# Optimization experiments

Hardware: AMD Instinct MI355X
Metric: run time of the kernel (lower is better)

The kernel has to match this reference:

```python
import jax, jax.numpy as jnp
import numpy as np

LAMBDA_TEMP = 20.0
GAMMA = 20.0
MARGIN = 0.05
EPS = 1e-8

B, K, M, D = 128, 256, 8, 128


def _unit(x, axis=-1):
    return x / jnp.linalg.norm(x, axis=axis, keepdims=True)


def setup_inputs() -> dict:
    key = jax.random.key(0)
    k1, k2, k3 = jax.random.split(key, 3)
    v_proj = _unit(jax.random.normal(k1, (B, K, D), dtype=jnp.float32))
    prototypes = _unit(jax.random.normal(k2, (K, M, D), dtype=jnp.float32))
    concept_labels = jax.random.randint(k3, (B, K), 0, 2, dtype=jnp.int64)
    return {"v_proj": v_proj, "concept_labels": concept_labels, "prototypes": prototypes}


def reference(v_proj, concept_labels, prototypes):
    # all-pairs prototype similarities: query vector (b,k) vs prototypes of concept c
    # sims: (B, K, C, M)
    sims = jnp.einsum('bkd,cmd->bkcm', v_proj, prototypes)
    # Eq.6: soft assignment over the M prototypes of each concept
    q = jax.nn.softmax(GAMMA * sims, axis=-1)
    # Eq.7-8: weighted similarity sim_c(v)  -> (B, K, C)
    sim = jnp.sum(q * sims, axis=-1)
    # positive similarity: concept k queried against its own prototypes, plus margin
    sim_pos = jnp.einsum('bkk->bk', sim) + MARGIN  # (B, K)
    # Eq.9: -log( exp(lam*sim_pos) / (sum_c exp(lam*sim_c) + eps) )
    denom = jnp.sum(jnp.exp(LAMBDA_TEMP * sim), axis=-1) + EPS  # (B, K)
    loss_bk = jnp.log(denom) - LAMBDA_TEMP * sim_pos  # (B, K)
    mask = (concept_labels == 1).astype(loss_bk.dtype)
    num_pos = jnp.sum(mask)
    total = jnp.sum(loss_bk * mask)
    return jnp.where(num_pos > 0, total / num_pos, total)
```

## Files before the change

kernel.cpp:

```cpp
#include <hip/hip_runtime.h>

#define NROWS 32768
#define LT 20.0f
#define CHUNKS 16

typedef _Float16 half8 __attribute__((ext_vector_type(8)));
typedef float    f32x4 __attribute__((ext_vector_type(4)));

__device__ __forceinline__ float swz16(float x) {
    return __int_as_float(__builtin_amdgcn_ds_swizzle(__float_as_int(x), 0x401F));
}

#define GLD16(gp, lp) __builtin_amdgcn_global_load_lds( \
    (const __attribute__((address_space(1))) void*)(gp), \
    (__attribute__((address_space(3))) void*)(lp), 16, 0, 0)

__global__ __launch_bounds__(256)
void mpcl_prep(const float* __restrict__ P, _Float16* __restrict__ Pw)
{
    int id   = blockIdx.x * 256 + threadIdx.x;
    int gcol = id >> 4;
    int dblk = id & 15;
    int ch   = gcol >> 7;
    int col  = gcol & 127;
    int key  = (col & 3) | ((col & 8) >> 1);
    int dbs  = (dblk & 8) | ((dblk ^ key) & 7);
    const float* src = P + (size_t)gcol * 128 + dblk * 8;
    float4 a = *(const float4*)src;
    float4 b = *(const float4*)(src + 4);
    half8 hv;
    hv[0] = (_Float16)a.x; hv[1] = (_Float16)a.y;
    hv[2] = (_Float16)a.z; hv[3] = (_Float16)a.w;
    hv[4] = (_Float16)b.x; hv[5] = (_Float16)b.y;
    hv[6] = (_Float16)b.z; hv[7] = (_Float16)b.w;
    *(half8*)&Pw[((size_t)ch * 2048 + col * 16 + dbs) * 8] = hv;
}

__global__ __launch_bounds__(1024)
void mpcl_main(const float* __restrict__ V,
               const int*   __restrict__ labels,
               const _Float16* __restrict__ Pw,
               int* __restrict__ ws,
               float* __restrict__ out)
{
    __shared__ __align__(16) _Float16 Pst[2][2048 * 8];
    __shared__ float sh_denom[128];
    __shared__ float sh_simpos[128];
    __shared__ float sh_red[32];

    int*   gcnt = ws;
    float* gsum = (float*)(ws + 2);

    const int tid  = threadIdx.x;
    const int lane = tid & 63;
    const int w    = tid >> 6;
    const int rg   = w >> 2;
    const int colq = w & 3;
    const int n    = lane & 15;
    const int q    = lane >> 4;
    const int rowbase = blockIdx.x * 128;

    if (tid < 128) { sh_denom[tid] = 0.0f; sh_simpos[tid] = 0.0f; }

    half8 vh[2][4];
#pragma unroll
    for (int rf = 0; rf < 2; ++rf) {
        const float* vr = V + (size_t)(rowbase + rg * 32 + rf * 16 + n) * 128 + q * 8;
#pragma unroll
        for (int c = 0; c < 4; ++c) {
            float4 x0 = *(const float4*)(vr + c * 32);
            float4 x1 = *(const float4*)(vr + c * 32 + 4);
            vh[rf][c][0] = (_Float16)x0.x; vh[rf][c][1] = (_Float16)x0.y;
            vh[rf][c][2] = (_Float16)x0.z; vh[rf][c][3] = (_Float16)x0.w;
            vh[rf][c][4] = (_Float16)x1.x; vh[rf][c][5] = (_Float16)x1.y;
            vh[rf][c][6] = (_Float16)x1.z; vh[rf][c][7] = (_Float16)x1.w;
        }
    }

    const int col1 = colq * 32 + ((n >> 2) << 3) + (n & 3);
    int off1[4];
#pragma unroll
    for (int c = 0; c < 4; ++c) {
        int dblk = c * 4 + q;
        int dbs  = (dblk & 8) | ((dblk ^ (n & 7)) & 7);
        off1[c]  = (col1 * 16 + dbs) * 8;
    }

    const _Float16* gbase = Pw + (size_t)(w * 128 + lane) * 8;
    _Float16* l0 = &Pst[0][(w * 128) * 8];
    _Float16* l1 = &Pst[1][(w * 128) * 8];

    GLD16(gbase,       l0);
    GLD16(gbase + 512, l0 + 512);

    const int rowk0 = (rowbase + rg * 32 + n) & 255;
    const int rowk1 = (rowbase + rg * 32 + 16 + n) & 255;

    float dn[2] = {0.f, 0.f};

#pragma unroll 1
    for (int ch = 0; ch < CHUNKS; ++ch) {
        __syncthreads();

        if (ch < CHUNKS - 1) {
            const _Float16* g = gbase + (size_t)(ch + 1) * 16384;
            _Float16* lnx = (ch & 1) ? l0 : l1;
            GLD16(g,       lnx);
            GLD16(g + 512, lnx + 512);
        }

        const _Float16* base = (ch & 1) ? &Pst[1][0] : &Pst[0][0];

        f32x4 acc1[2] = {{0.f,0.f,0.f,0.f},{0.f,0.f,0.f,0.f}};
        f32x4 acc2[2] = {{0.f,0.f,0.f,0.f},{0.f,0.f,0.f,0.f}};
#pragma unroll
        for (int c = 0; c < 4; ++c) {
            half8 a1 = *(const half8*)&base[off1[c]];
            half8 a2 = *(const half8*)&base[off1[c] + 512];
            acc1[0] = __builtin_amdgcn_mfma_f32_16x16x32_f16(a1, vh[0][c], acc1[0], 0, 0, 0);
            acc1[1] = __builtin_amdgcn_mfma_f32_16x16x32_f16(a1, vh[1][c], acc1[1], 0, 0, 0);
            acc2[0] = __builtin_amdgcn_mfma_f32_16x16x32_f16(a2, vh[0][c], acc2[0], 0, 0, 0);
            acc2[1] = __builtin_amdgcn_mfma_f32_16x16x32_f16(a2, vh[1][c], acc2[1], 0, 0, 0);
        }

        const int cA = ch * 16 + colq * 4 + q;
#pragma unroll
        for (int rf = 0; rf < 2; ++rf) {
            float x0 = acc1[rf][0], x1 = acc1[rf][1], x2 = acc1[rf][2], x3 = acc1[rf][3];
            float x4 = acc2[rf][0], x5 = acc2[rf][1], x6 = acc2[rf][2], x7 = acc2[rf][3];
            float e0 = __expf(LT * x0), e1 = __expf(LT * x1);
            float e2 = __expf(LT * x2), e3 = __expf(LT * x3);
            float e4 = __expf(LT * x4), e5 = __expf(LT * x5);
            float e6 = __expf(LT * x6), e7 = __expf(LT * x7);
            float es = ((e0 + e1) + (e2 + e3)) + ((e4 + e5) + (e6 + e7));
            float ss = fmaf(e0, x0, fmaf(e1, x1, fmaf(e2, x2, e3 * x3)))
                     + fmaf(e4, x4, fmaf(e5, x5, fmaf(e6, x6, e7 * x7)));
            float simc = __fdividef(ss, es);
            dn[rf] += __expf(LT * simc);
            if (cA == (rf ? rowk1 : rowk0))
                sh_simpos[rg * 32 + rf * 16 + n] = simc;
        }
    }

#pragma unroll
    for (int rf = 0; rf < 2; ++rf) {
        float t = dn[rf];
        t += swz16(t);
        t += __shfl_xor(t, 32);
        if (lane < 16)
            atomicAdd(&sh_denom[rg * 32 + rf * 16 + n], t);
    }
    __syncthreads();

    float s = 0.f, cc = 0.f;
    if (tid < 128) {
        int row = rowbase + tid;
        float lp = logf(sh_denom[tid] + 1e-8f) - LT * (sh_simpos[tid] + 0.05f);
        float mk = (labels[row] == 1) ? 1.0f : 0.0f;
        s = lp * mk;
        cc = mk;
    }
#pragma unroll
    for (int off = 32; off >= 1; off >>= 1) {
        s  += __shfl_down(s, off);
        cc += __shfl_down(cc, off);
    }
    if (lane == 0) { sh_red[w] = s; sh_red[16 + w] = cc; }
    __syncthreads();
    if (tid == 0) {
        s = 0.f; cc = 0.f;
#pragma unroll
        for (int i = 0; i < 16; ++i) { s += sh_red[i]; cc += sh_red[16 + i]; }
        atomicAdd(&gsum[0], s);
        atomicAdd(&gsum[1], cc);
        __threadfence();
        int g = __hip_atomic_fetch_add(gcnt, 1,
                                       __ATOMIC_ACQ_REL, __HIP_MEMORY_SCOPE_AGENT);
        if (g == 255) {
            __threadfence();
            float ts = __hip_atomic_load(&gsum[0], __ATOMIC_RELAXED, __HIP_MEMORY_SCOPE_AGENT);
            float tc = __hip_atomic_load(&gsum[1], __ATOMIC_RELAXED, __HIP_MEMORY_SCOPE_AGENT);
            out[0] = (tc > 0.0f) ? (ts / tc) : ts;
        }
    }
}

extern "C" void kernel_launch(void* const* d_in, const int* in_sizes, int n_in,
                              void* d_out, int out_size, void* d_ws, size_t ws_size,
                              hipStream_t stream)
{
    const float* V      = (const float*)d_in[0];
    const int*   labels = (const int*)d_in[1];
    const float* P      = (const float*)d_in[2];
    float* out = (float*)d_out;
    int*   ws  = (int*)d_ws;
    _Float16* Pw = (_Float16*)((char*)d_ws + 512);

    hipMemsetAsync(ws, 0, 16, stream);
    mpcl_prep<<<128, 256, 0, stream>>>(P, Pw);
    mpcl_main<<<256, 1024, 0, stream>>>(V, labels, Pw, ws, out);
}
```

Measured before the change: 109.5 us.

## Load prototypes straight to registers in fragment order, drop LDS staging and memset

```diff
diff --git a/kernel.cpp b/kernel.cpp
--- a/kernel.cpp
+++ b/kernel.cpp
@@ -1,31 +1,38 @@
 #include <hip/hip_runtime.h>
 
-#define NROWS 32768
-#define LT 20.0f
+#define LT     20.0f
+#define C2EXP  28.853900817779268f
 #define CHUNKS 16
+#define NBLK   512
 
 typedef _Float16 half8 __attribute__((ext_vector_type(8)));
 typedef float    f32x4 __attribute__((ext_vector_type(4)));
 
+#if __has_builtin(__builtin_amdgcn_exp2f)
+#define EXP2F(x) __builtin_amdgcn_exp2f(x)
+#else
+#define EXP2F(x) __expf(0.69314718055994531f * (x))
+#endif
+
 __device__ __forceinline__ float swz16(float x) {
     return __int_as_float(__builtin_amdgcn_ds_swizzle(__float_as_int(x), 0x401F));
 }
 
-#define GLD16(gp, lp) __builtin_amdgcn_global_load_lds( \
-    (const __attribute__((address_space(1))) void*)(gp), \
-    (__attribute__((address_space(3))) void*)(lp), 16, 0, 0)
-
 __global__ __launch_bounds__(256)
-void mpcl_prep(const float* __restrict__ P, _Float16* __restrict__ Pw)
+void mpcl_prep(const float* __restrict__ P, _Float16* __restrict__ Pw,
+               int* __restrict__ ws)
 {
-    int id   = blockIdx.x * 256 + threadIdx.x;
-    int gcol = id >> 4;
-    int dblk = id & 15;
-    int ch   = gcol >> 7;
-    int col  = gcol & 127;
-    int key  = (col & 3) | ((col & 8) >> 1);
-    int dbs  = (dblk & 8) | ((dblk ^ key) & 7);
-    const float* src = P + (size_t)gcol * 128 + dblk * 8;
+    int id = blockIdx.x * 256 + threadIdx.x;
+    if (id == 0) ws[0] = 0;
+    int ch    = id >> 11;
+    int colq  = (id >> 9) & 3;
+    int cfrag = (id >> 6) & 7;
+    int lane  = id & 63;
+    int n = lane & 15, q = lane >> 4;
+    int c = cfrag & 3, h = cfrag >> 2;
+    int col  = colq * 32 + ((n >> 2) << 3) + (n & 3) + (h << 2);
+    int gcol = (ch << 7) + col;
+    const float* src = P + ((size_t)gcol << 7) + c * 32 + q * 8;
     float4 a = *(const float4*)src;
     float4 b = *(const float4*)(src + 4);
     half8 hv;
@@ -33,39 +40,42 @@
     hv[2] = (_Float16)a.z; hv[3] = (_Float16)a.w;
     hv[4] = (_Float16)b.x; hv[5] = (_Float16)b.y;
     hv[6] = (_Float16)b.z; hv[7] = (_Float16)b.w;
-    *(half8*)&Pw[((size_t)ch * 2048 + col * 16 + dbs) * 8] = hv;
-}
-
-__global__ __launch_bounds__(1024)
+    *(half8*)(Pw + (size_t)id * 8) = hv;
+}
+
+__global__ __launch_bounds__(512, 4)
 void mpcl_main(const float* __restrict__ V,
                const int*   __restrict__ labels,
                const _Float16* __restrict__ Pw,
                int* __restrict__ ws,
                float* __restrict__ out)
 {
-    __shared__ __align__(16) _Float16 Pst[2][2048 * 8];
-    __shared__ float sh_denom[128];
-    __shared__ float sh_simpos[128];
-    __shared__ float sh_red[32];
+    __shared__ float sh_denom[64];
+    __shared__ float sh_simpos[64];
+    __shared__ float sh_fin[16];
+    __shared__ int   sh_last;
 
     int*   gcnt = ws;
-    float* gsum = (float*)(ws + 2);
+    float* part = (float*)((char*)ws + 256);
 
     const int tid  = threadIdx.x;
     const int lane = tid & 63;
     const int w    = tid >> 6;
+    const int colq = w & 3;
     const int rg   = w >> 2;
-    const int colq = w & 3;
     const int n    = lane & 15;
     const int q    = lane >> 4;
-    const int rowbase = blockIdx.x * 128;
-
-    if (tid < 128) { sh_denom[tid] = 0.0f; sh_simpos[tid] = 0.0f; }
+    const int rowbase = blockIdx.x * 64;
+
+    if (tid < 64) { sh_denom[tid] = 0.0f; sh_simpos[tid] = 0.0f; }
+
+    int lab = 0;
+    if (tid < 64) lab = labels[rowbase + tid];
 
     half8 vh[2][4];
 #pragma unroll
     for (int rf = 0; rf < 2; ++rf) {
-        const float* vr = V + (size_t)(rowbase + rg * 32 + rf * 16 + n) * 128 + q * 8;
+        const float* vr = V + ((size_t)(rowbase + rg * 32 + rf * 16 + n) << 7) + q * 8;
 #pragma unroll
         for (int c = 0; c < 4; ++c) {
             float4 x0 = *(const float4*)(vr + c * 32);
@@ -76,75 +86,67 @@
             vh[rf][c][6] = (_Float16)x1.z; vh[rf][c][7] = (_Float16)x1.w;
         }
     }
-
-    const int col1 = colq * 32 + ((n >> 2) << 3) + (n & 3);
-    int off1[4];
-#pragma unroll
-    for (int c = 0; c < 4; ++c) {
-        int dblk = c * 4 + q;
-        int dbs  = (dblk & 8) | ((dblk ^ (n & 7)) & 7);
-        off1[c]  = (col1 * 16 + dbs) * 8;
-    }
-
-    const _Float16* gbase = Pw + (size_t)(w * 128 + lane) * 8;
-    _Float16* l0 = &Pst[0][(w * 128) * 8];
-    _Float16* l1 = &Pst[1][(w * 128) * 8];
-
-    GLD16(gbase,       l0);
-    GLD16(gbase + 512, l0 + 512);
+    __syncthreads();
+
+    const half8* pw = (const half8*)Pw + (size_t)colq * 512 + lane;
 
     const int rowk0 = (rowbase + rg * 32 + n) & 255;
     const int rowk1 = (rowbase + rg * 32 + 16 + n) & 255;
 
-    float dn[2] = {0.f, 0.f};
-
+    float dn0 = 0.f, dn1 = 0.f;
+
+    half8 bufA[8], bufB[8];
+#pragma unroll
+    for (int f = 0; f < 8; ++f) bufA[f] = pw[f * 64];
+
+#define COMPUTE(BUF, CABASE) do {                                               \
+    f32x4 acc1[2] = {{0.f,0.f,0.f,0.f},{0.f,0.f,0.f,0.f}};                      \
+    f32x4 acc2[2] = {{0.f,0.f,0.f,0.f},{0.f,0.f,0.f,0.f}};                      \
+    _Pragma("unroll")                                                           \
+    for (int c = 0; c < 4; ++c) {                                               \
+        acc1[0] = __builtin_amdgcn_mfma_f32_16x16x32_f16(BUF[c],   vh[0][c], acc1[0], 0, 0, 0); \
+        acc1[1] = __builtin_amdgcn_mfma_f32_16x16x32_f16(BUF[c],   vh[1][c], acc1[1], 0, 0, 0); \
+        acc2[0] = __builtin_amdgcn_mfma_f32_16x16x32_f16(BUF[4+c], vh[0][c], acc2[0], 0, 0, 0); \
+        acc2[1] = __builtin_amdgcn_mfma_f32_16x16x32_f16(BUF[4+c], vh[1][c], acc2[1], 0, 0, 0); \
+    }                                                                           \
+    _Pragma("unroll")                                                           \
+    for (int rf = 0; rf < 2; ++rf) {                                            \
+        float x0 = acc1[rf][0], x1 = acc1[rf][1], x2 = acc1[rf][2], x3 = acc1[rf][3]; \
+        float x4 = acc2[rf][0], x5 = acc2[rf][1], x6 = acc2[rf][2], x7 = acc2[rf][3]; \
+        float e0 = EXP2F(C2EXP * x0), e1 = EXP2F(C2EXP * x1);                   \
+        float e2 = EXP2F(C2EXP * x2), e3 = EXP2F(C2EXP * x3);                   \
+        float e4 = EXP2F(C2EXP * x4), e5 = EXP2F(C2EXP * x5);                   \
+        float e6 = EXP2F(C2EXP * x6), e7 = EXP2F(C2EXP * x7);                   \
+        float es = ((e0 + e1) + (e2 + e3)) + ((e4 + e5) + (e6 + e7));           \
+        float ss = fmaf(e0, x0, fmaf(e1, x1, fmaf(e2, x2, e3 * x3)))            \
+                 + fmaf(e4, x4, fmaf(e5, x5, fmaf(e6, x6, e7 * x7)));           \
+        float simc = __fdividef(ss, es);                                        \
+        if (rf) dn1 += EXP2F(C2EXP * simc); else dn0 += EXP2F(C2EXP * simc);    \
+        if ((CABASE) == (rf ? rowk1 : rowk0))                                   \
+            sh_simpos[rg * 32 + rf * 16 + n] = simc;         \
+    }                                                                           \
+} while (0)
+
+    int cA = colq * 4 + q;
 #pragma unroll 1
-    for (int ch = 0; ch < CHUNKS; ++ch) {
-        __syncthreads();
-
-        if (ch < CHUNKS - 1) {
-            const _Float16* g = gbase + (size_t)(ch + 1) * 16384;
-            _Float16* lnx = (ch & 1) ? l0 : l1;
-            GLD16(g,       lnx);
-            GLD16(g + 512, lnx + 512);
-        }
-
-        const _Float16* base = (ch & 1) ? &Pst[1][0] : &Pst[0][0];
-
-        f32x4 acc1[2] = {{0.f,0.f,0.f,0.f},{0.f,0.f,0.f,0.f}};
-        f32x4 acc2[2] = {{0.f,0.f,0.f,0.f},{0.f,0.f,0.f,0.f}};
-#pragma unroll
-        for (int c = 0; c < 4; ++c) {
-            half8 a1 = *(const half8*)&base[off1[c]];
-            half8 a2 = *(const half8*)&base[off1[c] + 512];
-            acc1[0] = __builtin_amdgcn_mfma_f32_16x16x32_f16(a1, vh[0][c], acc1[0], 0, 0, 0);
-            acc1[1] = __builtin_amdgcn_mfma_f32_16x16x32_f16(a1, vh[1][c], acc1[1], 0, 0, 0);
-            acc2[0] = __builtin_amdgcn_mfma_f32_16x16x32_f16(a2, vh[0][c], acc2[0], 0, 0, 0);
-            acc2[1] = __builtin_amdgcn_mfma_f32_16x16x32_f16(a2, vh[1][c], acc2[1], 0, 0, 0);
-        }
-
-        const int cA = ch * 16 + colq * 4 + q;
-#pragma unroll
-        for (int rf = 0; rf < 2; ++rf) {
-            float x0 = acc1[rf][0], x1 = acc1[rf][1], x2 = acc1[rf][2], x3 = acc1[rf][3];
-            float x4 = acc2[rf][0], x5 = acc2[rf][1], x6 = acc2[rf][2], x7 = acc2[rf][3];
-            float e0 = __expf(LT * x0), e1 = __expf(LT * x1);
-            float e2 = __expf(LT * x2), e3 = __expf(LT * x3);
-            float e4 = __expf(LT * x4), e5 = __expf(LT * x5);
-            float e6 = __expf(LT * x6), e7 = __expf(LT * x7);
-            float es = ((e0 + e1) + (e2 + e3)) + ((e4 + e5) + (e6 + e7));
-            float ss = fmaf(e0, x0, fmaf(e1, x1, fmaf(e2, x2, e3 * x3)))
-                     + fmaf(e4, x4, fmaf(e5, x5, fmaf(e6, x6, e7 * x7)));
-            float simc = __fdividef(ss, es);
-            dn[rf] += __expf(LT * simc);
-            if (cA == (rf ? rowk1 : rowk0))
-                sh_simpos[rg * 32 + rf * 16 + n] = simc;
-        }
+    for (int ch = 0; ch < CHUNKS; ch += 2) {
+#pragma unroll
+        for (int f = 0; f < 8; ++f) bufB[f] = pw[(ch + 1) * 2048 + f * 64];
+
+        COMPUTE(bufA, cA);
+
+        if (ch + 2 < CHUNKS) {
+#pragma unroll
+            for (int f = 0; f < 8; ++f) bufA[f] = pw[(ch + 2) * 2048 + f * 64];
+        }
+
+        COMPUTE(bufB, cA + 16);
+        cA += 32;
     }
 
 #pragma unroll
     for (int rf = 0; rf < 2; ++rf) {
-        float t = dn[rf];
+        float t = rf ? dn1 : dn0;
         t += swz16(t);
         t += __shfl_xor(t, 32);
         if (lane < 16)
@@ -153,10 +155,9 @@
     __syncthreads();
 
     float s = 0.f, cc = 0.f;
-    if (tid < 128) {
-        int row = rowbase + tid;
+    if (tid < 64) {
         float lp = logf(sh_denom[tid] + 1e-8f) - LT * (sh_simpos[tid] + 0.05f);
-        float mk = (labels[row] == 1) ? 1.0f : 0.0f;
+        float mk = (lab == 1) ? 1.0f : 0.0f;
         s = lp * mk;
         cc = mk;
     }
@@ -165,21 +166,32 @@
         s  += __shfl_down(s, off);
         cc += __shfl_down(cc, off);
     }
-    if (lane == 0) { sh_red[w] = s; sh_red[16 + w] = cc; }
+
+    if (tid == 0) {
+        __hip_atomic_store(&part[2 * blockIdx.x],     s,  __ATOMIC_RELAXED, __HIP_MEMORY_SCOPE_AGENT);
+        __hip_atomic_store(&part[2 * blockIdx.x + 1], cc, __ATOMIC_RELAXED, __HIP_MEMORY_SCOPE_AGENT);
+        __threadfence();
+        int g = __hip_atomic_fetch_add(gcnt, 1, __ATOMIC_ACQ_REL, __HIP_MEMORY_SCOPE_AGENT);
+        sh_last = (g == NBLK - 1);
+    }
     __syncthreads();
-    if (tid == 0) {
-        s = 0.f; cc = 0.f;
-#pragma unroll
-        for (int i = 0; i < 16; ++i) { s += sh_red[i]; cc += sh_red[16 + i]; }
-        atomicAdd(&gsum[0], s);
-        atomicAdd(&gsum[1], cc);
-        __threadfence();
-        int g = __hip_atomic_fetch_add(gcnt, 1,
-                                       __ATOMIC_ACQ_REL, __HIP_MEMORY_SCOPE_AGENT);
-        if (g == 255) {
-            __threadfence();
-            float ts = __hip_atomic_load(&gsum[0], __ATOMIC_RELAXED, __HIP_MEMORY_SCOPE_AGENT);
-            float tc = __hip_atomic_load(&gsum[1], __ATOMIC_RELAXED, __HIP_MEMORY_SCOPE_AGENT);
+    if (sh_last) {
+        float ts = 0.f, tc = 0.f;
+        for (int i = tid; i < NBLK; i += 512) {
+            ts += __hip_atomic_load(&part[2 * i],     __ATOMIC_RELAXED, __HIP_MEMORY_SCOPE_AGENT);
+            tc += __hip_atomic_load(&part[2 * i + 1], __ATOMIC_RELAXED, __HIP_MEMORY_SCOPE_AGENT);
+        }
+#pragma unroll
+        for (int off = 32; off >= 1; off >>= 1) {
+            ts += __shfl_down(ts, off);
+            tc += __shfl_down(tc, off);
+        }
+        if (lane == 0) { sh_fin[w] = ts; sh_fin[8 + w] = tc; }
+        __syncthreads();
+        if (tid == 0) {
+            ts = 0.f; tc = 0.f;
+#pragma unroll
+            for (int i = 0; i < 8; ++i) { ts += sh_fin[i]; tc += sh_fin[8 + i]; }
             out[0] = (tc > 0.0f) ? (ts / tc) : ts;
         }
     }
@@ -194,9 +206,8 @@
     const float* P      = (const float*)d_in[2];
     float* out = (float*)d_out;
     int*   ws  = (int*)d_ws;
-    _Float16* Pw = (_Float16*)((char*)d_ws + 512);
-
-    hipMemsetAsync(ws, 0, 16, stream);
-    mpcl_prep<<<128, 256, 0, stream>>>(P, Pw);
-    mpcl_main<<<256, 1024, 0, stream>>>(V, labels, Pw, ws, out);
-}
+    _Float16* Pw = (_Float16*)((char*)d_ws + 16384);
+
+    mpcl_prep<<<128, 256, 0, stream>>>(P, Pw, ws);
+    mpcl_main<<<NBLK, 512, 0, stream>>>(V, labels, Pw, ws, out);
+}
```

Result: slower. 111.7 us (+2.0%).
